# Optimization experiments

Hardware: AMD Instinct MI355X
Metric: run time of the kernel (lower is better)

Reference implementation:

```python
import jax, jax.numpy as jnp
import numpy as np
import math

B, IN, D, H, DEPTH, E, K = 16384, 128, 512, 8, 3, 8, 2
FF, EH = 4 * D, 256          # ffn width = 4*d_model; expert hidden fixed at 256 in source
EPSILON = 0.1                # forward() default epsilon (exploration mixing)
LN_EPS = 1e-5


def _ln(x, w, b):
    m = x.mean(-1, keepdims=True)
    v = x.var(-1, keepdims=True)  # biased variance, matching nn.LayerNorm
    return (x - m) / jnp.sqrt(v + LN_EPS) * w + b


def setup_inputs() -> dict:
    key = jax.random.key(0)
    ks = jax.random.split(key, 16)
    s = 0.02
    rn = lambda k, shape: jax.random.normal(k, shape, jnp.float32) * s
    return dict(
        x=jax.random.normal(ks[0], (B, IN), jnp.float32),
        embed_w=rn(ks[1], (IN, D)), embed_b=jnp.zeros((D,), jnp.float32),
        ln1_w=jnp.ones((DEPTH, D), jnp.float32), ln1_b=jnp.zeros((DEPTH, D), jnp.float32),
        inproj_w=rn(ks[2], (DEPTH, 3 * D, D)), inproj_b=jnp.zeros((DEPTH, 3 * D), jnp.float32),
        outproj_w=rn(ks[3], (DEPTH, D, D)), outproj_b=jnp.zeros((DEPTH, D), jnp.float32),
        ln2_w=jnp.ones((DEPTH, D), jnp.float32), ln2_b=jnp.zeros((DEPTH, D), jnp.float32),
        ffn_w1=rn(ks[4], (DEPTH, D, FF)), ffn_b1=jnp.zeros((DEPTH, FF), jnp.float32),
        ffn_w2=rn(ks[5], (DEPTH, FF, D)), ffn_b2=jnp.zeros((DEPTH, D), jnp.float32),
        router_w=rn(ks[6], (D, E)), router_b=jnp.zeros((E,), jnp.float32),
        exp_w1=rn(ks[7], (E, D, EH)), exp_b1=jnp.zeros((E, EH), jnp.float32),
        exp_w2=rn(ks[8], (E, EH, D)), exp_b2=jnp.zeros((E, D), jnp.float32),
        head_ln_w=jnp.ones((D,), jnp.float32), head_ln_b=jnp.zeros((D,), jnp.float32),
        head_w=rn(ks[9], (D, 1)), head_b=jnp.zeros((1,), jnp.float32),
    )


def reference(x, embed_w, embed_b, ln1_w, ln1_b, inproj_w, inproj_b,
              outproj_w, outproj_b, ln2_w, ln2_b, ffn_w1, ffn_b1, ffn_w2, ffn_b2,
              router_w, router_b, exp_w1, exp_b1, exp_w2, exp_b2,
              head_ln_w, head_ln_b, head_w, head_b):
    h = x @ embed_w + embed_b                       # [B, D]; unsqueeze(1) -> seq_len == 1
    for l in range(DEPTH):
        g = _ln(h, ln1_w[l], ln1_b[l])
        qkv = g @ inproj_w[l].T + inproj_b[l]       # [B, 3D]
        # seq_len == 1: softmax over the single key is exactly 1, so attn(h,h,h) == out_proj(V)
        v = qkv[:, 2 * D:]
        a = v @ outproj_w[l].T + outproj_b[l]
        h = h + a
        g = _ln(h, ln2_w[l], ln2_b[l])
        h = h + jax.nn.gelu(g @ ffn_w1[l] + ffn_b1[l], approximate=False) @ ffn_w2[l] + ffn_b2[l]
    z = h                                           # squeeze(1)

    # WaggleGate
    logits = z @ router_w + router_b                # [B, E]
    probs = jax.nn.softmax(logits, axis=-1)
    probs = (1.0 - EPSILON) * probs + EPSILON / E
    wts, idx = jax.lax.top_k(probs, K)              # [B, K]
    load = probs.mean(0)
    aux = (load * jnp.log(load * E + 1e-9)).sum() / math.log(E + 1e-9)

    # dense all-expert compute + sparse top-k combine (same math as per-sample dispatch)
    hmid = jax.nn.gelu(jnp.einsum('bd,edh->ebh', z, exp_w1) + exp_b1[:, None, :], approximate=False)
    eo = jnp.einsum('ebh,ehd->ebd', hmid, exp_w2) + exp_b2[:, None, :]   # [E, B, D]
    gate = jnp.zeros((z.shape[0], E), z.dtype).at[
        jnp.arange(z.shape[0])[:, None], idx].add(wts)                    # [B, E]
    moe = jnp.einsum('be,ebd->bd', gate, eo)

    z = z + moe
    logit = (_ln(z, head_ln_w, head_ln_b) @ head_w + head_b)[:, 0]       # [B]
    return logit, aux
```

## Files before the change

kernel.cpp:

```cpp
#include <hip/hip_runtime.h>
#include <hip/hip_bf16.h>

#define B_TOK 16384
#define IN_DIM 128
#define D_DIM 512
#define DEPTH 3
#define NEXP 8
#define FF_DIM 2048
#define EH_DIM 256
#define MAXSLOT 33792
#define MAXTILE 264
#define NHBLK 64

typedef __attribute__((ext_vector_type(8))) __bf16 bf16x8;
typedef __attribute__((ext_vector_type(4))) float f32x4;
typedef __attribute__((ext_vector_type(4))) unsigned short u16x4;
typedef __attribute__((ext_vector_type(8))) unsigned short u16x8;

__device__ __forceinline__ unsigned short f2bf(float f){
    unsigned int u = __float_as_uint(f);
    u += 0x7fffu + ((u >> 16) & 1u);
    return (unsigned short)(u >> 16);
}
__device__ __forceinline__ float bf2f(unsigned short u){
    return __uint_as_float(((unsigned int)u) << 16);
}
__device__ __forceinline__ float geluf(float x){
    return 0.5f * x * (1.0f + erff(x * 0.70710678118654752f));
}
__device__ __forceinline__ void gload_lds16(const void* g, void* l){
    __builtin_amdgcn_global_load_lds((const __attribute__((address_space(1))) unsigned int*)g,
                                     (__attribute__((address_space(3))) unsigned int*)l,
                                     16, 0, 0);
}
__device__ __forceinline__ int xcd_swizzle(int orig, int nwg){
    const int q = nwg >> 3, r = nwg & 7;
    const int xcd = orig & 7;
    const int idx = orig >> 3;
    return (xcd < r ? xcd*(q+1) : r*(q+1) + (xcd-r)*q) + idx;
}

__global__ void zero_kernel(int* a, int na, int* b, int nb){
    const int i = blockIdx.x * blockDim.x + threadIdx.x;
    if (i < na) a[i] = 0;
    if (i < nb) b[i] = 0;
}

struct ConvSeg { const float* src; unsigned short* dst; int n4; };
struct ConvArgs { ConvSeg seg[2]; };

__global__ void convert_kernel(ConvArgs a){
    const int stride = gridDim.x * blockDim.x;
    const int tid = blockIdx.x * blockDim.x + threadIdx.x;
    for (int s = 0; s < 2; ++s){
        const f32x4* src = (const f32x4*)a.seg[s].src;
        u16x4* dst = (u16x4*)a.seg[s].dst;
        const int n4 = a.seg[s].n4;
        for (int i = tid; i < n4; i += stride){
            f32x4 v = src[i];
            u16x4 o;
            o[0] = f2bf(v[0]); o[1] = f2bf(v[1]); o[2] = f2bf(v[2]); o[3] = f2bf(v[3]);
            dst[i] = o;
        }
    }
}

struct TSeg { const float* src; unsigned short* dst; int K; int N; int tileStart; };
struct TArgs { TSeg seg[26]; };

__global__ void transpose_kernel(TArgs a){
    __shared__ float t[32][33];
    const int tile = blockIdx.x;
    int s = 0;
    #pragma unroll 1
    while (s < 25 && tile >= a.seg[s+1].tileStart) ++s;
    const TSeg sg = a.seg[s];
    const int local = tile - sg.tileStart;
    const int tilesN = sg.N >> 5;
    const int k0 = (local / tilesN) << 5;
    const int n0 = (local % tilesN) << 5;
    const int tx = threadIdx.x & 31;
    const int ty = threadIdx.x >> 5;
    #pragma unroll
    for (int j = 0; j < 4; ++j)
        t[ty + j*8][tx] = sg.src[(size_t)(k0 + ty + j*8) * sg.N + n0 + tx];
    __syncthreads();
    #pragma unroll
    for (int j = 0; j < 4; ++j){
        const int n = ty + j*8;
        sg.dst[(size_t)(n0 + n) * sg.K + k0 + tx] = f2bf(t[tx][n]);
    }
}

__global__ void foldb_kernel(const float* __restrict__ outproj_w, const float* __restrict__ outproj_b,
                             const float* __restrict__ inproj_b, float* __restrict__ bfold){
    const int l = blockIdx.x, n = threadIdx.x;
    const float* Wo = outproj_w + ((size_t)l*D_DIM + n)*D_DIM;
    const float* bv = inproj_b + l*3*D_DIM + 2*D_DIM;
    float acc = outproj_b[l*D_DIM + n];
    for (int j = 0; j < D_DIM; ++j) acc += Wo[j]*bv[j];
    bfold[l*D_DIM + n] = acc;
}

#define EPI_BF16 0
#define EPI_BF16_GELU 1
#define EPI_F32_BIAS 2
#define EPI_F32_RESID 3

template<int EPI>
__global__ void __launch_bounds__(256, 2)
gemm_bt(const unsigned short* __restrict__ A, const unsigned short* __restrict__ Bt,
        const float* __restrict__ bias, const float* __restrict__ resid,
        void* __restrict__ out, int NB, int N, int K)
{
    __shared__ unsigned short sh[32768];
    const int nwg = gridDim.x;
    const int wg  = xcd_swizzle(blockIdx.x, nwg);
    const int bn  = wg % NB;
    const int bm  = wg / NB;

    const int tid  = threadIdx.x;
    const int lane = tid & 63;
    const int wave = tid >> 6;
    const int wm = (wave >> 1) << 6;
    const int wn = (wave & 1) << 6;

    f32x4 acc[4][4] = {};

    const unsigned short* Abase = A + (size_t)bm * 128 * K;
    const unsigned short* Bbase = Bt + (size_t)bn * 128 * K;
    const int soff = tid * 16;

    auto STAGE = [&](int b, int kt){
        char* Ab = (char*)(sh + b*16384);
        char* Bb = (char*)(sh + b*16384 + 8192);
        #pragma unroll
        for (int s = 0; s < 4; ++s){
            const int off = s*4096 + soff;
            const int row = off >> 7, colb = off & 127;
            gload_lds16((const char*)(Abase + (size_t)row*K + kt) + colb, Ab + off);
        }
        #pragma unroll
        for (int s = 0; s < 4; ++s){
            const int off = s*4096 + soff;
            const int row = off >> 7, colb = off & 127;
            gload_lds16((const char*)(Bbase + (size_t)row*K + kt) + colb, Bb + off);
        }
    };
    auto COMPUTE = [&](int b){
        const unsigned short* Ab = sh + b*16384;
        const unsigned short* Bb = sh + b*16384 + 8192;
        #pragma unroll
        for (int ks = 0; ks < 2; ++ks){
            const int k0 = ks*32 + ((lane>>4)<<3);
            bf16x8 af[4], bfr[4];
            #pragma unroll
            for (int i=0;i<4;i++) af[i]  = *(const bf16x8*)&Ab[(wm + i*16 + (lane&15))*64 + k0];
            #pragma unroll
            for (int j=0;j<4;j++) bfr[j] = *(const bf16x8*)&Bb[(wn + j*16 + (lane&15))*64 + k0];
            #pragma unroll
            for (int i=0;i<4;i++)
                #pragma unroll
                for (int j=0;j<4;j++)
                    acc[i][j] = __builtin_amdgcn_mfma_f32_16x16x32_bf16(af[i], bfr[j], acc[i][j], 0, 0, 0);
        }
    };

    STAGE(0, 0);
    __syncthreads();
    const int nk = K >> 6;
    int cur = 0;
    for (int i = 0; i < nk; ++i){
        if (i + 1 < nk) STAGE(cur ^ 1, (i + 1) << 6);
        COMPUTE(cur);
        __syncthreads();
        cur ^= 1;
    }

    const int r0 = ((lane>>4)<<2);
    const int cc = lane & 15;

    if (EPI == EPI_F32_BIAS || EPI == EPI_F32_RESID){
        #pragma unroll
        for (int j=0;j<4;j++){
            const int col = bn*128 + wn + j*16 + cc;
            const float bv = bias[col];
            #pragma unroll
            for (int i=0;i<4;i++){
                #pragma unroll
                for (int r=0;r<4;r++){
                    const int row = bm*128 + wm + i*16 + r0 + r;
                    const size_t idx = (size_t)row * N + col;
                    float v = acc[i][j][r] + bv;
                    if (EPI == EPI_F32_BIAS) ((float*)out)[idx] = v;
                    else                     ((float*)out)[idx] = resid[idx] + v;
                }
            }
        }
    } else {
        unsigned short* Ct = sh;
        float bcol[4];
        #pragma unroll
        for (int j=0;j<4;j++) bcol[j] = bias[bn*128 + wn + j*16 + cc];
        #pragma unroll
        for (int i=0;i<4;i++){
            #pragma unroll
            for (int r=0;r<4;r++){
                const int rl = wm + i*16 + r0 + r;
                #pragma unroll
                for (int j=0;j<4;j++){
                    float v = acc[i][j][r] + bcol[j];
                    if (EPI == EPI_BF16_GELU) v = geluf(v);
                    Ct[rl*128 + wn + j*16 + cc] = f2bf(v);
                }
            }
        }
        __syncthreads();
        const int orow = tid >> 4;
        const int ocol = (tid & 15) * 8;
        unsigned short* op = (unsigned short*)out;
        #pragma unroll
        for (int p = 0; p < 8; ++p){
            const int row = p*16 + orow;
            *(u16x4*)(&op[(size_t)(bm*128 + row)*N + bn*128 + ocol])     = *(u16x4*)&Ct[row*128 + ocol];
            *(u16x4*)(&op[(size_t)(bm*128 + row)*N + bn*128 + ocol + 4]) = *(u16x4*)&Ct[row*128 + ocol + 4];
        }
    }
}

#define MEPI_GELU 0
#define MEPI_GATED 1

template<int MEPI, int INDIRECT>
__global__ void __launch_bounds__(256, 2)
gemm_moe(const unsigned short* __restrict__ A, const int* __restrict__ tok,
         const int* __restrict__ offs, const unsigned short* __restrict__ wbase,
         int wstride, const float* __restrict__ bbase, int bstride,
         const float* __restrict__ gslot, unsigned short* __restrict__ out,
         int NB, int N, int K)
{
    __shared__ unsigned short sh[32768];
    const int nwg = gridDim.x;
    const int wg  = xcd_swizzle(blockIdx.x, nwg);
    const int bn  = wg % NB;
    const int bm  = wg / NB;
    const int m0  = bm * 128;
    if (m0 >= offs[8]) return;

    const int tid  = threadIdx.x;
    const int lane = tid & 63;
    const int wave = tid >> 6;
    const int wm = (wave >> 1) << 6;
    const int wn = (wave & 1) << 6;

    int e = 0;
    #pragma unroll 1
    while (offs[e+1] <= m0) ++e;

    const unsigned short* Bt = wbase + (size_t)e*wstride;
    const float* bias = bbase + (size_t)e*bstride;

    f32x4 acc[4][4] = {};
    const int soff = tid * 16;

    const unsigned short* Arow[4];
    int colb_[4];
    #pragma unroll
    for (int s = 0; s < 4; ++s){
        const int off = s*4096 + soff;
        const int row = off >> 7;
        colb_[s] = off & 127;
        if (INDIRECT){
            const int t = tok[m0 + row];
            Arow[s] = A + (size_t)t*K;
        } else {
            Arow[s] = A + (size_t)(m0 + row)*K;
        }
    }
    const unsigned short* Bbase = Bt + (size_t)bn * 128 * K;

    auto STAGE = [&](int b, int kt){
        char* Ab = (char*)(sh + b*16384);
        char* Bb = (char*)(sh + b*16384 + 8192);
        #pragma unroll
        for (int s = 0; s < 4; ++s){
            const int off = s*4096 + soff;
            gload_lds16((const char*)(Arow[s] + kt) + colb_[s], Ab + off);
        }
        #pragma unroll
        for (int s = 0; s < 4; ++s){
            const int off = s*4096 + soff;
            const int row = off >> 7, colb = off & 127;
            gload_lds16((const char*)(Bbase + (size_t)row*K + kt) + colb, Bb + off);
        }
    };
    auto COMPUTE = [&](int b){
        const unsigned short* Ab = sh + b*16384;
        const unsigned short* Bb = sh + b*16384 + 8192;
        #pragma unroll
        for (int ks = 0; ks < 2; ++ks){
            const int k0 = ks*32 + ((lane>>4)<<3);
            bf16x8 af[4], bfr[4];
            #pragma unroll
            for (int i=0;i<4;i++) af[i]  = *(const bf16x8*)&Ab[(wm + i*16 + (lane&15))*64 + k0];
            #pragma unroll
            for (int j=0;j<4;j++) bfr[j] = *(const bf16x8*)&Bb[(wn + j*16 + (lane&15))*64 + k0];
            #pragma unroll
            for (int i=0;i<4;i++)
                #pragma unroll
                for (int j=0;j<4;j++)
                    acc[i][j] = __builtin_amdgcn_mfma_f32_16x16x32_bf16(af[i], bfr[j], acc[i][j], 0, 0, 0);
        }
    };

    STAGE(0, 0);
    __syncthreads();
    const int nk = K >> 6;
    int cur = 0;
    for (int i = 0; i < nk; ++i){
        if (i + 1 < nk) STAGE(cur ^ 1, (i + 1) << 6);
        COMPUTE(cur);
        __syncthreads();
        cur ^= 1;
    }

    const int r0 = ((lane>>4)<<2);
    const int cc = lane & 15;
    unsigned short* Ct = sh;
    float bcol[4];
    #pragma unroll
    for (int j=0;j<4;j++) bcol[j] = bias[bn*128 + wn + j*16 + cc];
    #pragma unroll
    for (int i=0;i<4;i++){
        #pragma unroll
        for (int r=0;r<4;r++){
            const int rl = wm + i*16 + r0 + r;
            float g = 1.0f;
            if (MEPI == MEPI_GATED) g = gslot[m0 + rl];
            #pragma unroll
            for (int j=0;j<4;j++){
                float v = acc[i][j][r] + bcol[j];
                if (MEPI == MEPI_GELU) v = geluf(v);
                else                   v = v * g;
                Ct[rl*128 + wn + j*16 + cc] = f2bf(v);
            }
        }
    }
    __syncthreads();
    const int orow = tid >> 4;
    const int ocol = (tid & 15) * 8;
    #pragma unroll
    for (int p = 0; p < 8; ++p){
        const int row = p*16 + orow;
        *(u16x4*)(&out[(size_t)(m0 + row)*N + bn*128 + ocol])     = *(u16x4*)&Ct[row*128 + ocol];
        *(u16x4*)(&out[(size_t)(m0 + row)*N + bn*128 + ocol + 4]) = *(u16x4*)&Ct[row*128 + ocol + 4];
    }
}

__global__ void ln_kernel(const float* __restrict__ x, const float* __restrict__ w,
                          const float* __restrict__ b, unsigned short* __restrict__ out)
{
    const int lane = threadIdx.x & 63;
    const int wave = threadIdx.x >> 6;
    const int row  = blockIdx.x * 4 + wave;
    const float* xr = x + (size_t)row * D_DIM;
    f32x4 v0 = *(const f32x4*)(xr + lane*8);
    f32x4 v1 = *(const f32x4*)(xr + lane*8 + 4);
    float s  = v0[0]+v0[1]+v0[2]+v0[3] + v1[0]+v1[1]+v1[2]+v1[3];
    float s2 = v0[0]*v0[0]+v0[1]*v0[1]+v0[2]*v0[2]+v0[3]*v0[3]
             + v1[0]*v1[0]+v1[1]*v1[1]+v1[2]*v1[2]+v1[3]*v1[3];
    #pragma unroll
    for (int o = 32; o > 0; o >>= 1){ s += __shfl_xor(s, o); s2 += __shfl_xor(s2, o); }
    const float mean = s * (1.0f/512.0f);
    const float var  = s2 * (1.0f/512.0f) - mean*mean;
    const float inv  = 1.0f / sqrtf(var + 1e-5f);
    const int k = lane*8;
    u16x4 o0, o1;
    #pragma unroll
    for (int j=0;j<4;j++) o0[j] = f2bf((v0[j]-mean)*inv*w[k+j]   + b[k+j]);
    #pragma unroll
    for (int j=0;j<4;j++) o1[j] = f2bf((v1[j]-mean)*inv*w[k+4+j] + b[k+4+j]);
    *(u16x4*)(out + (size_t)row*D_DIM + k)     = o0;
    *(u16x4*)(out + (size_t)row*D_DIM + k + 4) = o1;
}

__global__ void router_kernel(const float* __restrict__ z, const float* __restrict__ rw,
                              const float* __restrict__ rb, unsigned short* __restrict__ zbf,
                              int2* __restrict__ idx2, float2* __restrict__ wts2,
                              float* __restrict__ bsums)
{
    __shared__ float ps[4][8];
    const int lane = threadIdx.x & 63;
    const int wave = threadIdx.x >> 6;
    const int row  = blockIdx.x * 4 + wave;
    const float* zr = z + (size_t)row * D_DIM;
    f32x4 z0 = *(const f32x4*)(zr + lane*8);
    f32x4 z1 = *(const f32x4*)(zr + lane*8 + 4);
    {
        u16x4 o0, o1;
        #pragma unroll
        for (int j=0;j<4;j++){ o0[j] = f2bf(z0[j]); o1[j] = f2bf(z1[j]); }
        *(u16x4*)(zbf + (size_t)row*D_DIM + lane*8)     = o0;
        *(u16x4*)(zbf + (size_t)row*D_DIM + lane*8 + 4) = o1;
    }
    float acc[8] = {0,0,0,0,0,0,0,0};
    #pragma unroll
    for (int j = 0; j < 8; ++j){
        const float zv = (j < 4) ? z0[j] : z1[j-4];
        const float* wr = rw + (size_t)(lane*8 + j) * 8;
        f32x4 w0 = *(const f32x4*)wr;
        f32x4 w1 = *(const f32x4*)(wr + 4);
        acc[0] += zv*w0[0]; acc[1] += zv*w0[1]; acc[2] += zv*w0[2]; acc[3] += zv*w0[3];
        acc[4] += zv*w1[0]; acc[5] += zv*w1[1]; acc[6] += zv*w1[2]; acc[7] += zv*w1[3];
    }
    #pragma unroll
    for (int o = 32; o > 0; o >>= 1){
        #pragma unroll
        for (int e = 0; e < 8; ++e) acc[e] += __shfl_xor(acc[e], o);
    }
    if (lane == 0){
        float p[8]; float mx = -1e30f;
        #pragma unroll
        for (int e=0;e<8;e++){ p[e] = acc[e] + rb[e]; mx = fmaxf(mx, p[e]); }
        float se = 0.f;
        #pragma unroll
        for (int e=0;e<8;e++){ p[e] = expf(p[e]-mx); se += p[e]; }
        const float sc = 0.9f / se;
        #pragma unroll
        for (int e=0;e<8;e++) p[e] = p[e]*sc + 0.0125f;
        int i1 = 0;
        #pragma unroll
        for (int e=1;e<8;e++) if (p[e] > p[i1]) i1 = e;
        int i2 = (i1 == 0) ? 1 : 0;
        for (int e=i2+1;e<8;e++) if (e != i1 && p[e] > p[i2]) i2 = e;
        idx2[row] = make_int2(i1, i2);
        wts2[row] = make_float2(p[i1], p[i2]);
        #pragma unroll
        for (int e=0;e<8;e++) ps[wave][e] = p[e];
    }
    __syncthreads();
    if (threadIdx.x < 8){
        bsums[blockIdx.x*8 + threadIdx.x] =
            ps[0][threadIdx.x] + ps[1][threadIdx.x] + ps[2][threadIdx.x] + ps[3][threadIdx.x];
    }
}

__global__ void hist_kernel(const int2* __restrict__ idx2, int* __restrict__ blockHist){
    __shared__ int hc[8];
    if (threadIdx.x < 8) hc[threadIdx.x] = 0;
    __syncthreads();
    const int t = blockIdx.x * 256 + threadIdx.x;
    const int2 ii = idx2[t];
    atomicAdd(&hc[ii.x], 1);
    atomicAdd(&hc[ii.y], 1);
    __syncthreads();
    if (threadIdx.x < 8) blockHist[blockIdx.x*8 + threadIdx.x] = hc[threadIdx.x];
}

__global__ void scan_kernel(const int* __restrict__ blockHist, int* __restrict__ offs,
                            int* __restrict__ baseArr){
    if (threadIdx.x == 0){
        int counts[8];
        #pragma unroll
        for (int e=0;e<8;e++) counts[e] = 0;
        for (int b=0;b<NHBLK;b++)
            #pragma unroll
            for (int e=0;e<8;e++) counts[e] += blockHist[b*8+e];
        int o = 0; offs[0] = 0;
        int start[8];
        #pragma unroll
        for (int e=0;e<8;e++){ start[e] = o; o += (counts[e]+127)&~127; offs[e+1] = o; }
        for (int e=0;e<8;e++){
            int cur = start[e];
            for (int b=0;b<NHBLK;b++){ baseArr[b*8+e] = cur; cur += blockHist[b*8+e]; }
        }
    }
}

__global__ void assign_kernel(const int2* __restrict__ idx2, const float2* __restrict__ wts2,
                              const int* __restrict__ baseArr, int2* __restrict__ slot_map,
                              float* __restrict__ gslot, int* __restrict__ tok)
{
    __shared__ int cur[8];
    if (threadIdx.x < 8) cur[threadIdx.x] = 0;
    __syncthreads();
    const int t = blockIdx.x * 256 + threadIdx.x;
    const int2 ii = idx2[t];
    const float2 ww = wts2[t];
    const int r1 = atomicAdd(&cur[ii.x], 1);
    const int r2 = atomicAdd(&cur[ii.y], 1);
    const int s1 = baseArr[blockIdx.x*8 + ii.x] + r1;
    const int s2 = baseArr[blockIdx.x*8 + ii.y] + r2;
    slot_map[t] = make_int2(s1, s2);
    gslot[s1] = ww.x; gslot[s2] = ww.y;
    tok[s1] = t; tok[s2] = t;
}

__global__ void aux_kernel(const float* __restrict__ bsums, float* __restrict__ out_aux)
{
    __shared__ float part[256];
    const int t = threadIdx.x;
    const int e = t & 7, chunk = t >> 3;
    float s = 0.f;
    for (int blk = chunk*128; blk < chunk*128 + 128; ++blk) s += bsums[blk*8 + e];
    part[t] = s;
    __syncthreads();
    if (t < 8){
        float tot = 0.f;
        for (int c = 0; c < 32; ++c) tot += part[c*8 + t];
        part[t] = tot;
    }
    __syncthreads();
    if (t == 0){
        float aux = 0.f;
        for (int e2 = 0; e2 < 8; ++e2){
            float load = part[e2] * (1.0f/16384.0f);
            aux += load * logf(load * 8.0f + 1e-9f);
        }
        out_aux[0] = aux / 2.0794415416798357f;
    }
}

__global__ void head_kernel(const float* __restrict__ h, const unsigned short* __restrict__ eog,
                            const int2* __restrict__ slot_map,
                            const float* __restrict__ w, const float* __restrict__ b,
                            const float* __restrict__ hw, const float* __restrict__ hb,
                            float* __restrict__ out)
{
    const int lane = threadIdx.x & 63;
    const int wave = threadIdx.x >> 6;
    const int row  = blockIdx.x * 4 + wave;
    const int2 sm = slot_map[row];
    const float* zr = h + (size_t)row * D_DIM;
    f32x4 v0 = *(const f32x4*)(zr + lane*8);
    f32x4 v1 = *(const f32x4*)(zr + lane*8 + 4);
    u16x8 e1 = *(const u16x8*)(eog + (size_t)sm.x * D_DIM + lane*8);
    u16x8 e2 = *(const u16x8*)(eog + (size_t)sm.y * D_DIM + lane*8);
    #pragma unroll
    for (int j=0;j<4;j++){ v0[j] += bf2f(e1[j]) + bf2f(e2[j]); }
    #pragma unroll
    for (int j=0;j<4;j++){ v1[j] += bf2f(e1[4+j]) + bf2f(e2[4+j]); }
    float s  = v0[0]+v0[1]+v0[2]+v0[3] + v1[0]+v1[1]+v1[2]+v1[3];
    float s2 = v0[0]*v0[0]+v0[1]*v0[1]+v0[2]*v0[2]+v0[3]*v0[3]
             + v1[0]*v1[0]+v1[1]*v1[1]+v1[2]*v1[2]+v1[3]*v1[3];
    #pragma unroll
    for (int o = 32; o > 0; o >>= 1){ s += __shfl_xor(s, o); s2 += __shfl_xor(s2, o); }
    const float mean = s * (1.0f/512.0f);
    const float var  = s2 * (1.0f/512.0f) - mean*mean;
    const float inv  = 1.0f / sqrtf(var + 1e-5f);
    const int k = lane*8;
    float dot = 0.f;
    #pragma unroll
    for (int j=0;j<4;j++) dot += ((v0[j]-mean)*inv*w[k+j]   + b[k+j])   * hw[k+j];
    #pragma unroll
    for (int j=0;j<4;j++) dot += ((v1[j]-mean)*inv*w[k+4+j] + b[k+4+j]) * hw[k+4+j];
    #pragma unroll
    for (int o = 32; o > 0; o >>= 1) dot += __shfl_xor(dot, o);
    if (lane == 0) out[row] = dot + hb[0];
}

extern "C" void kernel_launch(void* const* d_in, const int* in_sizes, int n_in,
                              void* d_out, int out_size, void* d_ws, size_t ws_size,
                              hipStream_t stream)
{
    (void)in_sizes; (void)n_in; (void)out_size; (void)ws_size;
    const float* x         = (const float*)d_in[0];
    const float* embed_w   = (const float*)d_in[1];
    const float* embed_b   = (const float*)d_in[2];
    const float* ln1_w     = (const float*)d_in[3];
    const float* ln1_b     = (const float*)d_in[4];
    const float* inproj_w  = (const float*)d_in[5];
    const float* inproj_b  = (const float*)d_in[6];
    const float* outproj_w = (const float*)d_in[7];
    const float* outproj_b = (const float*)d_in[8];
    const float* ln2_w     = (const float*)d_in[9];
    const float* ln2_b     = (const float*)d_in[10];
    const float* ffn_w1    = (const float*)d_in[11];
    const float* ffn_b1    = (const float*)d_in[12];
    const float* ffn_w2    = (const float*)d_in[13];
    const float* ffn_b2    = (const float*)d_in[14];
    const float* router_w  = (const float*)d_in[15];
    const float* router_b  = (const float*)d_in[16];
    const float* exp_w1    = (const float*)d_in[17];
    const float* exp_b1    = (const float*)d_in[18];
    const float* exp_w2    = (const float*)d_in[19];
    const float* exp_b2    = (const float*)d_in[20];
    const float* head_ln_w = (const float*)d_in[21];
    const float* head_ln_b = (const float*)d_in[22];
    const float* head_w    = (const float*)d_in[23];
    const float* head_b    = (const float*)d_in[24];

    char* ws = (char*)d_ws;
    unsigned short* xbf   = (unsigned short*)(ws + 0);
    unsigned short* ebf   = (unsigned short*)(ws + 4194304);
    unsigned short* wobf  = (unsigned short*)(ws + 4325376);
    unsigned short* wvtbf = (unsigned short*)(ws + 5898240);
    unsigned short* wfold = (unsigned short*)(ws + 7471104);
    unsigned short* w1t   = (unsigned short*)(ws + 9043968);
    unsigned short* w2t   = (unsigned short*)(ws + 15335424);
    unsigned short* e1t   = (unsigned short*)(ws + 21626880);
    unsigned short* e2t   = (unsigned short*)(ws + 23724032);
    float*          h     = (float*)(ws + 25821184);
    unsigned short* gbf   = (unsigned short*)(ws + 59375616);
    unsigned short* ubf   = (unsigned short*)(ws + 76152832);
    unsigned short* hmidg = ubf;
    unsigned short* eog   = (unsigned short*)(ws + 93454336);
    char* MISC = ws + 143261696;
    int*    offs     = (int*)(MISC + 0);
    float*  zbias    = (float*)(MISC + 256);
    float*  bfold    = (float*)(MISC + 2304);
    int2*   idx2     = (int2*)(MISC + 8448);
    float2* wts2     = (float2*)(MISC + 139520);
    int2*   slot_map = (int2*)(MISC + 270592);
    float*  gslot    = (float*)(MISC + 401664);
    int*    tok      = (int*)(MISC + 536832);
    float*  bsums    = (float*)(MISC + 672000);
    int*    blockHist= (int*)(MISC + 803072);
    int*    baseArr  = (int*)(MISC + 805120);
    unsigned short* zbf = gbf;
    float* out = (float*)d_out;

    zero_kernel<<<(MAXSLOT + 255)/256, 256, 0, stream>>>((int*)zbias, 512, tok, MAXSLOT);

    ConvArgs ca;
    ca.seg[0] = { x, xbf, B_TOK*IN_DIM/4 };
    ca.seg[1] = { outproj_w, wobf, DEPTH*D_DIM*D_DIM/4 };
    convert_kernel<<<1024, 256, 0, stream>>>(ca);

    TArgs ta;
    int tcur = 0, ti = 0;
    ta.seg[ti] = { embed_w, ebf, IN_DIM, D_DIM, tcur };
    tcur += (IN_DIM/32)*(D_DIM/32); ++ti;
    for (int l = 0; l < DEPTH; ++l){
        ta.seg[ti] = { ffn_w1 + (size_t)l*D_DIM*FF_DIM, w1t + (size_t)l*FF_DIM*D_DIM, D_DIM, FF_DIM, tcur };
        tcur += (D_DIM/32)*(FF_DIM/32); ++ti;
    }
    for (int l = 0; l < DEPTH; ++l){
        ta.seg[ti] = { ffn_w2 + (size_t)l*FF_DIM*D_DIM, w2t + (size_t)l*D_DIM*FF_DIM, FF_DIM, D_DIM, tcur };
        tcur += (FF_DIM/32)*(D_DIM/32); ++ti;
    }
    for (int e = 0; e < NEXP; ++e){
        ta.seg[ti] = { exp_w1 + (size_t)e*D_DIM*EH_DIM, e1t + (size_t)e*EH_DIM*D_DIM, D_DIM, EH_DIM, tcur };
        tcur += (D_DIM/32)*(EH_DIM/32); ++ti;
    }
    for (int e = 0; e < NEXP; ++e){
        ta.seg[ti] = { exp_w2 + (size_t)e*EH_DIM*D_DIM, e2t + (size_t)e*D_DIM*EH_DIM, EH_DIM, D_DIM, tcur };
        tcur += (EH_DIM/32)*(D_DIM/32); ++ti;
    }
    for (int l = 0; l < DEPTH; ++l){
        ta.seg[ti] = { inproj_w + (size_t)l*3*D_DIM*D_DIM + 2*D_DIM*D_DIM,
                       wvtbf + (size_t)l*D_DIM*D_DIM, D_DIM, D_DIM, tcur };
        tcur += (D_DIM/32)*(D_DIM/32); ++ti;
    }
    transpose_kernel<<<tcur, 256, 0, stream>>>(ta);

    foldb_kernel<<<DEPTH, D_DIM, 0, stream>>>(outproj_w, outproj_b, inproj_b, bfold);

    const dim3 blk(256);
    for (int l = 0; l < DEPTH; ++l){
        gemm_bt<EPI_BF16><<<16, blk, 0, stream>>>(
            wobf + (size_t)l*D_DIM*D_DIM, wvtbf + (size_t)l*D_DIM*D_DIM,
            zbias, nullptr, wfold + (size_t)l*D_DIM*D_DIM, 4, D_DIM, D_DIM);
    }

    gemm_bt<EPI_F32_BIAS><<<(D_DIM/128)*(B_TOK/128), blk, 0, stream>>>(
        xbf, ebf, embed_b, nullptr, h, D_DIM/128, D_DIM, IN_DIM);

    for (int l = 0; l < DEPTH; ++l){
        ln_kernel<<<B_TOK/4, 256, 0, stream>>>(h, ln1_w + l*D_DIM, ln1_b + l*D_DIM, gbf);
        gemm_bt<EPI_F32_RESID><<<(D_DIM/128)*(B_TOK/128), blk, 0, stream>>>(
            gbf, wfold + (size_t)l*D_DIM*D_DIM, bfold + l*D_DIM, h, h, D_DIM/128, D_DIM, D_DIM);
        ln_kernel<<<B_TOK/4, 256, 0, stream>>>(h, ln2_w + l*D_DIM, ln2_b + l*D_DIM, gbf);
        gemm_bt<EPI_BF16_GELU><<<(FF_DIM/128)*(B_TOK/128), blk, 0, stream>>>(
            gbf, w1t + (size_t)l*FF_DIM*D_DIM, ffn_b1 + l*FF_DIM, nullptr, ubf, FF_DIM/128, FF_DIM, D_DIM);
        gemm_bt<EPI_F32_RESID><<<(D_DIM/128)*(B_TOK/128), blk, 0, stream>>>(
            ubf, w2t + (size_t)l*D_DIM*FF_DIM, ffn_b2 + l*D_DIM, h, h, D_DIM/128, D_DIM, FF_DIM);
    }

    router_kernel<<<B_TOK/4, 256, 0, stream>>>(h, router_w, router_b, zbf, idx2, wts2, bsums);
    aux_kernel<<<1, 256, 0, stream>>>(bsums, out + B_TOK);
    hist_kernel<<<NHBLK, 256, 0, stream>>>(idx2, blockHist);
    scan_kernel<<<1, 64, 0, stream>>>(blockHist, offs, baseArr);
    assign_kernel<<<NHBLK, 256, 0, stream>>>(idx2, wts2, baseArr, slot_map, gslot, tok);

    gemm_moe<MEPI_GELU, 1><<<(EH_DIM/128)*MAXTILE, blk, 0, stream>>>(
        zbf, tok, offs, e1t, EH_DIM*D_DIM, exp_b1, EH_DIM, nullptr, hmidg, EH_DIM/128, EH_DIM, D_DIM);
    gemm_moe<MEPI_GATED, 0><<<(D_DIM/128)*MAXTILE, blk, 0, stream>>>(
        hmidg, nullptr, offs, e2t, D_DIM*EH_DIM, exp_b2, D_DIM, gslot, eog, D_DIM/128, D_DIM, EH_DIM);

    head_kernel<<<B_TOK/4, 256, 0, stream>>>(h, eog, slot_map, head_ln_w, head_ln_b, head_w, head_b, out);
}
```

Baseline: 697.5 us.

## Replace FFN and MoE GEMMs with 256x128-tile 8-wave ping-pong kernel

Adds a gemm256 kernel that uses 256x128 output tiles, 512 threads and XOR-swizzled LDS staging. It double-buffers A and B in separate K-halves, issues loads asynchronously between MFMA phases, and raises wave priority around the MFMA blocks. This one kernel replaces the 128x128 dense FFN and attention-fold GEMMs as well as both MoE expert GEMMs. Expert segments are now padded to 256 rows, and the slot and workspace offsets are resized to match. The aim is more data reuse per tile and better overlap of loads with compute. In exchange it uses 96KB of LDS per block, which limits occupancy, and the extra padding adds wasted rows in the MoE GEMMs.

```diff
diff --git a/kernel.cpp b/kernel.cpp
--- a/kernel.cpp
+++ b/kernel.cpp
@@ -8,8 +8,8 @@
 #define NEXP 8
 #define FF_DIM 2048
 #define EH_DIM 256
-#define MAXSLOT 33792
-#define MAXTILE 264
+#define MAXSLOT 34816
+#define MAXT256 136
 #define NHBLK 64
 
 typedef __attribute__((ext_vector_type(8))) __bf16 bf16x8;
@@ -38,6 +38,11 @@
     const int xcd = orig & 7;
     const int idx = orig >> 3;
     return (xcd < r ? xcd*(q+1) : r*(q+1) + (xcd-r)*q) + idx;
+}
+__device__ __forceinline__ void wgbar(){
+    asm volatile("" ::: "memory");
+    __builtin_amdgcn_s_barrier();
+    asm volatile("" ::: "memory");
 }
 
 __global__ void zero_kernel(int* a, int na, int* b, int nb){
@@ -103,15 +108,12 @@
 }
 
 #define EPI_BF16 0
-#define EPI_BF16_GELU 1
 #define EPI_F32_BIAS 2
-#define EPI_F32_RESID 3
 
 template<int EPI>
 __global__ void __launch_bounds__(256, 2)
 gemm_bt(const unsigned short* __restrict__ A, const unsigned short* __restrict__ Bt,
-        const float* __restrict__ bias, const float* __restrict__ resid,
-        void* __restrict__ out, int NB, int N, int K)
+        const float* __restrict__ bias, void* __restrict__ out, int NB, int N, int K)
 {
     __shared__ unsigned short sh[32768];
     const int nwg = gridDim.x;
@@ -180,22 +182,18 @@
     const int r0 = ((lane>>4)<<2);
     const int cc = lane & 15;
 
-    if (EPI == EPI_F32_BIAS || EPI == EPI_F32_RESID){
+    if (EPI == EPI_F32_BIAS){
         #pragma unroll
         for (int j=0;j<4;j++){
             const int col = bn*128 + wn + j*16 + cc;
             const float bv = bias[col];
             #pragma unroll
-            for (int i=0;i<4;i++){
+            for (int i=0;i<4;i++)
                 #pragma unroll
                 for (int r=0;r<4;r++){
                     const int row = bm*128 + wm + i*16 + r0 + r;
-                    const size_t idx = (size_t)row * N + col;
-                    float v = acc[i][j][r] + bv;
-                    if (EPI == EPI_F32_BIAS) ((float*)out)[idx] = v;
-                    else                     ((float*)out)[idx] = resid[idx] + v;
+                    ((float*)out)[(size_t)row * N + col] = acc[i][j][r] + bv;
                 }
-            }
         }
     } else {
         unsigned short* Ct = sh;
@@ -203,18 +201,14 @@
         #pragma unroll
         for (int j=0;j<4;j++) bcol[j] = bias[bn*128 + wn + j*16 + cc];
         #pragma unroll
-        for (int i=0;i<4;i++){
+        for (int i=0;i<4;i++)
             #pragma unroll
             for (int r=0;r<4;r++){
                 const int rl = wm + i*16 + r0 + r;
                 #pragma unroll
-                for (int j=0;j<4;j++){
-                    float v = acc[i][j][r] + bcol[j];
-                    if (EPI == EPI_BF16_GELU) v = geluf(v);
-                    Ct[rl*128 + wn + j*16 + cc] = f2bf(v);
-                }
+                for (int j=0;j<4;j++)
+                    Ct[rl*128 + wn + j*16 + cc] = f2bf(acc[i][j][r] + bcol[j]);
             }
-        }
         __syncthreads();
         const int orow = tid >> 4;
         const int ocol = (tid & 15) * 8;
@@ -228,132 +222,225 @@
     }
 }
 
-#define MEPI_GELU 0
-#define MEPI_GATED 1
-
-template<int MEPI, int INDIRECT>
-__global__ void __launch_bounds__(256, 2)
-gemm_moe(const unsigned short* __restrict__ A, const int* __restrict__ tok,
-         const int* __restrict__ offs, const unsigned short* __restrict__ wbase,
-         int wstride, const float* __restrict__ bbase, int bstride,
-         const float* __restrict__ gslot, unsigned short* __restrict__ out,
-         int NB, int N, int K)
+#define G_GELU_BF16 0
+#define G_F32_RESID 1
+#define G_GATED_BF16 2
+#define ASZ 32768
+#define BSZ 16384
+
+template<int EPI, int MOE, int INDIRECT>
+__global__ void __launch_bounds__(512, 2)
+gemm256(const unsigned short* __restrict__ A, const unsigned short* __restrict__ BtG,
+        const float* __restrict__ biasG, const float* __restrict__ resid,
+        const int* __restrict__ tok, const int* __restrict__ offs,
+        int wstride, int bstride, const float* __restrict__ gslot,
+        void* __restrict__ out, int NB, int N, int K)
 {
-    __shared__ unsigned short sh[32768];
+    __shared__ __align__(16) char sh[98304];
     const int nwg = gridDim.x;
     const int wg  = xcd_swizzle(blockIdx.x, nwg);
     const int bn  = wg % NB;
     const int bm  = wg / NB;
-    const int m0  = bm * 128;
-    if (m0 >= offs[8]) return;
-
-    const int tid  = threadIdx.x;
-    const int lane = tid & 63;
-    const int wave = tid >> 6;
-    const int wm = (wave >> 1) << 6;
-    const int wn = (wave & 1) << 6;
-
-    int e = 0;
-    #pragma unroll 1
-    while (offs[e+1] <= m0) ++e;
-
-    const unsigned short* Bt = wbase + (size_t)e*wstride;
-    const float* bias = bbase + (size_t)e*bstride;
+    const int m0  = bm * 256;
+
+    const unsigned short* Bt = BtG;
+    const float* bias = biasG;
+    if (MOE){
+        if (m0 >= offs[8]) return;
+        int e = 0;
+        #pragma unroll 1
+        while (offs[e+1] <= m0) ++e;
+        Bt   += (size_t)e * wstride;
+        bias += (size_t)e * bstride;
+    }
+
+    const int tid = threadIdx.x, lane = tid & 63, wave = tid >> 6;
+    const int wm = (wave >> 1) * 64;
+    const int wn = (wave & 1) * 64;
+
+    const int srow = wave*16 + (lane >> 3);
+    const int scol = ((lane & 7) ^ (lane >> 3)) * 8;
+    const unsigned short* aptr[2][2];
+    #pragma unroll
+    for (int u = 0; u < 2; ++u)
+        #pragma unroll
+        for (int l = 0; l < 2; ++l){
+            const int r = u*128 + srow + l*8;
+            const int gr = INDIRECT ? tok[m0 + r] : (m0 + r);
+            aptr[u][l] = A + (size_t)gr * K + scol;
+        }
+    const unsigned short* bptr[2];
+    #pragma unroll
+    for (int l = 0; l < 2; ++l)
+        bptr[l] = Bt + (size_t)(bn*128 + srow + l*8) * K + scol;
+    const int sdst = wave*2048 + lane*16;
+
+    int aoff[2], boff[2];
+    #pragma unroll
+    for (int ks = 0; ks < 2; ++ks){
+        const int ch = (((ks<<2) + (lane>>4)) ^ (lane & 7)) << 4;
+        aoff[ks] = (wm + (lane & 15))*128 + ch;
+        boff[ks] = (wn + (lane & 15))*128 + ch;
+    }
 
     f32x4 acc[4][4] = {};
-    const int soff = tid * 16;
-
-    const unsigned short* Arow[4];
-    int colb_[4];
-    #pragma unroll
-    for (int s = 0; s < 4; ++s){
-        const int off = s*4096 + soff;
-        const int row = off >> 7;
-        colb_[s] = off & 127;
-        if (INDIRECT){
-            const int t = tok[m0 + row];
-            Arow[s] = A + (size_t)t*K;
+    bf16x8 bfr[4][2];
+
+    auto STA = [&](int buf, int kt){
+        #pragma unroll
+        for (int u = 0; u < 2; ++u)
+            #pragma unroll
+            for (int l = 0; l < 2; ++l)
+                gload_lds16(aptr[u][l] + kt, sh + buf*ASZ + u*16384 + l*1024 + sdst);
+    };
+    auto STB = [&](int buf, int kt){
+        #pragma unroll
+        for (int l = 0; l < 2; ++l)
+            gload_lds16(bptr[l] + kt, sh + 65536 + buf*BSZ + l*1024 + sdst);
+    };
+    auto RDB = [&](int buf){
+        #pragma unroll
+        for (int nf = 0; nf < 4; ++nf)
+            #pragma unroll
+            for (int ks = 0; ks < 2; ++ks)
+                bfr[nf][ks] = *(const bf16x8*)(sh + 65536 + buf*BSZ + nf*2048 + boff[ks]);
+    };
+
+    STA(0, 0);
+    STB(0, 0);
+    STB(1, 64);
+    asm volatile("s_waitcnt vmcnt(2)" ::: "memory");
+    wgbar();
+
+    const int NT = K >> 7;
+    for (int u = 0; u < NT; ++u){
+        const int kb = u << 7;
+        const bool more = (u + 1 < NT);
+        bf16x8 af[2][2];
+
+        RDB(0);
+        #pragma unroll
+        for (int m2 = 0; m2 < 2; ++m2)
+            #pragma unroll
+            for (int ks = 0; ks < 2; ++ks)
+                af[m2][ks] = *(const bf16x8*)(sh + 0*ASZ + (0+m2)*2048 + aoff[ks]);
+        STA(1, kb + 64);
+        wgbar();
+        __builtin_amdgcn_s_setprio(1);
+        #pragma unroll
+        for (int m2 = 0; m2 < 2; ++m2)
+            #pragma unroll
+            for (int nf = 0; nf < 4; ++nf)
+                #pragma unroll
+                for (int ks = 0; ks < 2; ++ks)
+                    acc[0+m2][nf] = __builtin_amdgcn_mfma_f32_16x16x32_bf16(af[m2][ks], bfr[nf][ks], acc[0+m2][nf], 0,0,0);
+        __builtin_amdgcn_s_setprio(0);
+        wgbar();
+
+        #pragma unroll
+        for (int m2 = 0; m2 < 2; ++m2)
+            #pragma unroll
+            for (int ks = 0; ks < 2; ++ks)
+                af[m2][ks] = *(const bf16x8*)(sh + 0*ASZ + (2+m2)*2048 + aoff[ks]);
+        if (more){
+            STB(0, kb + 128);
+            asm volatile("s_waitcnt vmcnt(2)" ::: "memory");
         } else {
-            Arow[s] = A + (size_t)(m0 + row)*K;
-        }
-    }
-    const unsigned short* Bbase = Bt + (size_t)bn * 128 * K;
-
-    auto STAGE = [&](int b, int kt){
-        char* Ab = (char*)(sh + b*16384);
-        char* Bb = (char*)(sh + b*16384 + 8192);
-        #pragma unroll
-        for (int s = 0; s < 4; ++s){
-            const int off = s*4096 + soff;
-            gload_lds16((const char*)(Arow[s] + kt) + colb_[s], Ab + off);
-        }
-        #pragma unroll
-        for (int s = 0; s < 4; ++s){
-            const int off = s*4096 + soff;
-            const int row = off >> 7, colb = off & 127;
-            gload_lds16((const char*)(Bbase + (size_t)row*K + kt) + colb, Bb + off);
-        }
-    };
-    auto COMPUTE = [&](int b){
-        const unsigned short* Ab = sh + b*16384;
-        const unsigned short* Bb = sh + b*16384 + 8192;
-        #pragma unroll
-        for (int ks = 0; ks < 2; ++ks){
-            const int k0 = ks*32 + ((lane>>4)<<3);
-            bf16x8 af[4], bfr[4];
-            #pragma unroll
-            for (int i=0;i<4;i++) af[i]  = *(const bf16x8*)&Ab[(wm + i*16 + (lane&15))*64 + k0];
-            #pragma unroll
-            for (int j=0;j<4;j++) bfr[j] = *(const bf16x8*)&Bb[(wn + j*16 + (lane&15))*64 + k0];
-            #pragma unroll
-            for (int i=0;i<4;i++)
-                #pragma unroll
-                for (int j=0;j<4;j++)
-                    acc[i][j] = __builtin_amdgcn_mfma_f32_16x16x32_bf16(af[i], bfr[j], acc[i][j], 0, 0, 0);
-        }
-    };
-
-    STAGE(0, 0);
-    __syncthreads();
-    const int nk = K >> 6;
-    int cur = 0;
-    for (int i = 0; i < nk; ++i){
-        if (i + 1 < nk) STAGE(cur ^ 1, (i + 1) << 6);
-        COMPUTE(cur);
+            asm volatile("s_waitcnt vmcnt(0)" ::: "memory");
+        }
+        wgbar();
+        __builtin_amdgcn_s_setprio(1);
+        #pragma unroll
+        for (int m2 = 0; m2 < 2; ++m2)
+            #pragma unroll
+            for (int nf = 0; nf < 4; ++nf)
+                #pragma unroll
+                for (int ks = 0; ks < 2; ++ks)
+                    acc[2+m2][nf] = __builtin_amdgcn_mfma_f32_16x16x32_bf16(af[m2][ks], bfr[nf][ks], acc[2+m2][nf], 0,0,0);
+        __builtin_amdgcn_s_setprio(0);
+        wgbar();
+
+        RDB(1);
+        #pragma unroll
+        for (int m2 = 0; m2 < 2; ++m2)
+            #pragma unroll
+            for (int ks = 0; ks < 2; ++ks)
+                af[m2][ks] = *(const bf16x8*)(sh + 1*ASZ + (0+m2)*2048 + aoff[ks]);
+        if (more) STA(0, kb + 128);
+        wgbar();
+        __builtin_amdgcn_s_setprio(1);
+        #pragma unroll
+        for (int m2 = 0; m2 < 2; ++m2)
+            #pragma unroll
+            for (int nf = 0; nf < 4; ++nf)
+                #pragma unroll
+                for (int ks = 0; ks < 2; ++ks)
+                    acc[0+m2][nf] = __builtin_amdgcn_mfma_f32_16x16x32_bf16(af[m2][ks], bfr[nf][ks], acc[0+m2][nf], 0,0,0);
+        __builtin_amdgcn_s_setprio(0);
+        wgbar();
+
+        #pragma unroll
+        for (int m2 = 0; m2 < 2; ++m2)
+            #pragma unroll
+            for (int ks = 0; ks < 2; ++ks)
+                af[m2][ks] = *(const bf16x8*)(sh + 1*ASZ + (2+m2)*2048 + aoff[ks]);
+        if (more) STB(1, kb + 192);
+        asm volatile("s_waitcnt vmcnt(2)" ::: "memory");
+        wgbar();
+        __builtin_amdgcn_s_setprio(1);
+        #pragma unroll
+        for (int m2 = 0; m2 < 2; ++m2)
+            #pragma unroll
+            for (int nf = 0; nf < 4; ++nf)
+                #pragma unroll
+                for (int ks = 0; ks < 2; ++ks)
+                    acc[2+m2][nf] = __builtin_amdgcn_mfma_f32_16x16x32_bf16(af[m2][ks], bfr[nf][ks], acc[2+m2][nf], 0,0,0);
+        __builtin_amdgcn_s_setprio(0);
+        wgbar();
+    }
+
+    const int r4 = (lane >> 4) * 4;
+    const int cc = lane & 15;
+    if (EPI == G_F32_RESID){
+        #pragma unroll
+        for (int nf = 0; nf < 4; ++nf){
+            const int col = bn*128 + wn + nf*16 + cc;
+            const float bv = bias[col];
+            #pragma unroll
+            for (int mf = 0; mf < 4; ++mf)
+                #pragma unroll
+                for (int r = 0; r < 4; ++r){
+                    const int row = m0 + wm + mf*16 + r4 + r;
+                    const size_t idx = (size_t)row * N + col;
+                    ((float*)out)[idx] = resid[idx] + acc[mf][nf][r] + bv;
+                }
+        }
+    } else {
+        unsigned short* ct = (unsigned short*)sh;
+        #pragma unroll
+        for (int nf = 0; nf < 4; ++nf){
+            const float bv = bias[bn*128 + wn + nf*16 + cc];
+            #pragma unroll
+            for (int mf = 0; mf < 4; ++mf)
+                #pragma unroll
+                for (int r = 0; r < 4; ++r){
+                    const int row = wm + mf*16 + r4 + r;
+                    float v = acc[mf][nf][r] + bv;
+                    if (EPI == G_GELU_BF16) v = geluf(v);
+                    else                    v *= gslot[m0 + row];
+                    ct[row*128 + wn + nf*16 + cc] = f2bf(v);
+                }
+        }
         __syncthreads();
-        cur ^= 1;
-    }
-
-    const int r0 = ((lane>>4)<<2);
-    const int cc = lane & 15;
-    unsigned short* Ct = sh;
-    float bcol[4];
-    #pragma unroll
-    for (int j=0;j<4;j++) bcol[j] = bias[bn*128 + wn + j*16 + cc];
-    #pragma unroll
-    for (int i=0;i<4;i++){
-        #pragma unroll
-        for (int r=0;r<4;r++){
-            const int rl = wm + i*16 + r0 + r;
-            float g = 1.0f;
-            if (MEPI == MEPI_GATED) g = gslot[m0 + rl];
-            #pragma unroll
-            for (int j=0;j<4;j++){
-                float v = acc[i][j][r] + bcol[j];
-                if (MEPI == MEPI_GELU) v = geluf(v);
-                else                   v = v * g;
-                Ct[rl*128 + wn + j*16 + cc] = f2bf(v);
-            }
-        }
-    }
-    __syncthreads();
-    const int orow = tid >> 4;
-    const int ocol = (tid & 15) * 8;
-    #pragma unroll
-    for (int p = 0; p < 8; ++p){
-        const int row = p*16 + orow;
-        *(u16x4*)(&out[(size_t)(m0 + row)*N + bn*128 + ocol])     = *(u16x4*)&Ct[row*128 + ocol];
-        *(u16x4*)(&out[(size_t)(m0 + row)*N + bn*128 + ocol + 4]) = *(u16x4*)&Ct[row*128 + ocol + 4];
+        unsigned short* op = (unsigned short*)out;
+        #pragma unroll
+        for (int p = 0; p < 8; ++p){
+            const int uidx = p*512 + tid;
+            const int row = uidx >> 4;
+            const int cu  = uidx & 15;
+            *(u16x8*)(op + (size_t)(m0 + row)*N + bn*128 + cu*8) =
+                *(const u16x8*)(ct + row*128 + cu*8);
+        }
     }
 }
 
@@ -469,7 +556,7 @@
         int o = 0; offs[0] = 0;
         int start[8];
         #pragma unroll
-        for (int e=0;e<8;e++){ start[e] = o; o += (counts[e]+127)&~127; offs[e+1] = o; }
+        for (int e=0;e<8;e++){ start[e] = o; o += (counts[e]+255)&~255; offs[e+1] = o; }
         for (int e=0;e<8;e++){
             int cur = start[e];
             for (int b=0;b<NHBLK;b++){ baseArr[b*8+e] = cur; cur += blockHist[b*8+e]; }
@@ -604,7 +691,7 @@
     unsigned short* gbf   = (unsigned short*)(ws + 59375616);
     unsigned short* ubf   = (unsigned short*)(ws + 76152832);
     unsigned short* hmidg = ubf;
-    unsigned short* eog   = (unsigned short*)(ws + 93454336);
+    unsigned short* eog   = (unsigned short*)(ws + 93978624);
     char* MISC = ws + 143261696;
     int*    offs     = (int*)(MISC + 0);
     float*  zbias    = (float*)(MISC + 256);
@@ -613,10 +700,10 @@
     float2* wts2     = (float2*)(MISC + 139520);
     int2*   slot_map = (int2*)(MISC + 270592);
     float*  gslot    = (float*)(MISC + 401664);
-    int*    tok      = (int*)(MISC + 536832);
-    float*  bsums    = (float*)(MISC + 672000);
-    int*    blockHist= (int*)(MISC + 803072);
-    int*    baseArr  = (int*)(MISC + 805120);
+    int*    tok      = (int*)(MISC + 544768);
+    float*  bsums    = (float*)(MISC + 684032);
+    int*    blockHist= (int*)(MISC + 815104);
+    int*    baseArr  = (int*)(MISC + 817152);
     unsigned short* zbf = gbf;
     float* out = (float*)d_out;
 
@@ -656,37 +743,41 @@
 
     foldb_kernel<<<DEPTH, D_DIM, 0, stream>>>(outproj_w, outproj_b, inproj_b, bfold);
 
-    const dim3 blk(256);
     for (int l = 0; l < DEPTH; ++l){
-        gemm_bt<EPI_BF16><<<16, blk, 0, stream>>>(
+        gemm_bt<EPI_BF16><<<16, 256, 0, stream>>>(
             wobf + (size_t)l*D_DIM*D_DIM, wvtbf + (size_t)l*D_DIM*D_DIM,
-            zbias, nullptr, wfold + (size_t)l*D_DIM*D_DIM, 4, D_DIM, D_DIM);
-    }
-
-    gemm_bt<EPI_F32_BIAS><<<(D_DIM/128)*(B_TOK/128), blk, 0, stream>>>(
-        xbf, ebf, embed_b, nullptr, h, D_DIM/128, D_DIM, IN_DIM);
+            zbias, wfold + (size_t)l*D_DIM*D_DIM, 4, D_DIM, D_DIM);
+    }
+
+    gemm_bt<EPI_F32_BIAS><<<(D_DIM/128)*(B_TOK/128), 256, 0, stream>>>(
+        xbf, ebf, embed_b, h, D_DIM/128, D_DIM, IN_DIM);
 
     for (int l = 0; l < DEPTH; ++l){
         ln_kernel<<<B_TOK/4, 256, 0, stream>>>(h, ln1_w + l*D_DIM, ln1_b + l*D_DIM, gbf);
-        gemm_bt<EPI_F32_RESID><<<(D_DIM/128)*(B_TOK/128), blk, 0, stream>>>(
-            gbf, wfold + (size_t)l*D_DIM*D_DIM, bfold + l*D_DIM, h, h, D_DIM/128, D_DIM, D_DIM);
+        gemm256<G_F32_RESID,0,0><<<(B_TOK/256)*(D_DIM/128), 512, 0, stream>>>(
+            gbf, wfold + (size_t)l*D_DIM*D_DIM, bfold + l*D_DIM, h,
+            nullptr, nullptr, 0, 0, nullptr, h, D_DIM/128, D_DIM, D_DIM);
         ln_kernel<<<B_TOK/4, 256, 0, stream>>>(h, ln2_w + l*D_DIM, ln2_b + l*D_DIM, gbf);
-        gemm_bt<EPI_BF16_GELU><<<(FF_DIM/128)*(B_TOK/128), blk, 0, stream>>>(
-            gbf, w1t + (size_t)l*FF_DIM*D_DIM, ffn_b1 + l*FF_DIM, nullptr, ubf, FF_DIM/128, FF_DIM, D_DIM);
-        gemm_bt<EPI_F32_RESID><<<(D_DIM/128)*(B_TOK/128), blk, 0, stream>>>(
-            ubf, w2t + (size_t)l*D_DIM*FF_DIM, ffn_b2 + l*D_DIM, h, h, D_DIM/128, D_DIM, FF_DIM);
+        gemm256<G_GELU_BF16,0,0><<<(B_TOK/256)*(FF_DIM/128), 512, 0, stream>>>(
+            gbf, w1t + (size_t)l*FF_DIM*D_DIM, ffn_b1 + l*FF_DIM, nullptr,
+            nullptr, nullptr, 0, 0, nullptr, ubf, FF_DIM/128, FF_DIM, D_DIM);
+        gemm256<G_F32_RESID,0,0><<<(B_TOK/256)*(D_DIM/128), 512, 0, stream>>>(
+            ubf, w2t + (size_t)l*D_DIM*FF_DIM, ffn_b2 + l*D_DIM, h,
+            nullptr, nullptr, 0, 0, nullptr, h, D_DIM/128, D_DIM, FF_DIM);
     }
 
     router_kernel<<<B_TOK/4, 256, 0, stream>>>(h, router_w, router_b, zbf, idx2, wts2, bsums);
     aux_kernel<<<1, 256, 0, stream>>>(bsums, out + B_TOK);
     hist_kernel<<<NHBLK, 256, 0, stream>>>(idx2, blockHist);
     scan_kernel<<<1, 64, 0, stream>>>(blockHist, offs, baseArr);
-    assign_kernel<<<NHBLK, 256, 0, stream>>>(idx2, wts2, baseArr, slot_map, gslot, tok);
-
-    gemm_moe<MEPI_GELU, 1><<<(EH_DIM/128)*MAXTILE, blk, 0, stream>>>(
-        zbf, tok, offs, e1t, EH_DIM*D_DIM, exp_b1, EH_DIM, nullptr, hmidg, EH_DIM/128, EH_DIM, D_DIM);
-    gemm_moe<MEPI_GATED, 0><<<(D_DIM/128)*MAXTILE, blk, 0, stream>>>(
-        hmidg, nullptr, offs, e2t, D_DIM*EH_DIM, exp_b2, D_DIM, gslot, eog, D_DIM/128, D_DIM, EH_DIM);
+    assign_kernel<<<B_TOK/256, 256, 0, stream>>>(idx2, wts2, baseArr, slot_map, gslot, tok);
+
+    gemm256<G_GELU_BF16,1,1><<<MAXT256*(EH_DIM/128), 512, 0, stream>>>(
+        zbf, e1t, exp_b1, nullptr, tok, offs, EH_DIM*D_DIM, EH_DIM, nullptr,
+        hmidg, EH_DIM/128, EH_DIM, D_DIM);
+    gemm256<G_GATED_BF16,1,0><<<MAXT256*(D_DIM/128), 512, 0, stream>>>(
+        hmidg, e2t, exp_b2, nullptr, nullptr, offs, D_DIM*EH_DIM, D_DIM, gslot,
+        eog, D_DIM/128, D_DIM, EH_DIM);
 
     head_kernel<<<B_TOK/4, 256, 0, stream>>>(h, eog, slot_map, head_ln_w, head_ln_b, head_w, head_b, out);
 }
```

Result: faster. 679.2 us (-2.6%).
